# Optimization experiments

Hardware: AMD Instinct MI355X
Metric: run time of the kernel (lower is better)

## Reference

```python
import jax, jax.numpy as jnp
import numpy as np

EMBED_DIM = 128
NUM_SYMBOLS = 100000
PAD_IDX = NUM_SYMBOLS
B = 8192
K = 50


def setup_inputs() -> dict:
    key = jax.random.key(0)
    ks = jax.random.split(key, 10)
    emb = jax.random.normal(ks[0], (NUM_SYMBOLS + 1, EMBED_DIM), jnp.float32) * 0.02
    emb = emb.at[PAD_IDX].set(0.0)  # padding_idx row is zero
    xav2 = 1.0 / np.sqrt(0.5 * (2 * EMBED_DIM + EMBED_DIM))
    xavg1 = 1.0 / np.sqrt(0.5 * (EMBED_DIM + EMBED_DIM // 2))
    xavg2 = 1.0 / np.sqrt(0.5 * (EMBED_DIM // 2 + 1))
    return {
        "entity": jax.random.randint(ks[1], (B,), 0, NUM_SYMBOLS),
        "connections": jax.random.randint(ks[2], (B, K, 2), 0, NUM_SYMBOLS),
        "symbol_emb": emb,
        "gcn_w_W": jax.random.normal(ks[3], (EMBED_DIM, 2 * EMBED_DIM), jnp.float32) * xav2,
        "gcn_w_b": jnp.zeros((EMBED_DIM,), jnp.float32),
        "gcn_b": jnp.zeros((EMBED_DIM,), jnp.float32),
        "gate_w1": jax.random.normal(ks[4], (EMBED_DIM // 2, EMBED_DIM), jnp.float32) * xavg1,
        "gate_b1": jnp.zeros((EMBED_DIM // 2,), jnp.float32),
        "gate_w2": jax.random.normal(ks[5], (1, EMBED_DIM // 2), jnp.float32) * xavg2,
        "gate_b2": jnp.zeros((1,), jnp.float32),
        "gate_temp": jnp.float32(1.0),
    }


def reference(entity, connections, symbol_emb, gcn_w_W, gcn_w_b, gcn_b,
              gate_w1, gate_b1, gate_w2, gate_b2, gate_temp):
    # Gather: center + (relation, entity) neighbor embeddings
    self_emb = symbol_emb[entity]                      # [B, D]
    rel = symbol_emb[connections[..., 0]]              # [B, K, D]
    ent = symbol_emb[connections[..., 1]]              # [B, K, D]
    # Linear transform of concatenated (rel, ent): gcn_w
    nbr = jnp.einsum('bkf,df->bkd', jnp.concatenate([rel, ent], axis=-1), gcn_w_W) + gcn_w_b  # [B, K, D]
    # Similarity attention (scaled dot product with center embedding)
    scores = jnp.einsum('bd,bkd->bk', self_emb, nbr) / jnp.sqrt(jnp.float32(EMBED_DIM))
    attn = jax.nn.softmax(scores, axis=-1)             # [B, K]
    # Content-based gating MLP (D -> D/2 -> 1), temperature-scaled sigmoid
    h = jax.nn.relu(jnp.einsum('bkd,hd->bkh', nbr, gate_w1) + gate_b1)
    gate = jax.nn.sigmoid((jnp.einsum('bkh,oh->bko', h, gate_w2) + gate_b2) / gate_temp)  # [B, K, 1]
    # Weight neighbors, aggregate='max' over k_neighbors, bias + tanh
    weighted = attn[..., None] * gate * nbr            # [B, K, D]
    out = jnp.max(weighted, axis=1)                    # [B, D]
    return jnp.tanh(out + gcn_b)
```

## Files before the change

### kernel.cpp

```cpp
#include <hip/hip_runtime.h>

#define EMBED_D 128
#define KNBR 50
#define STR 136
#define NROWS 102
#define ZK 50
#define NTF 52
#define XSTR 264
#define NSTR 136
#define MROWS 64

typedef __attribute__((ext_vector_type(8))) short short8;
typedef __attribute__((ext_vector_type(4))) float floatx4;

__device__ __forceinline__ float b2f(unsigned short u) {
    union { unsigned int i; float f; } v;
    v.i = ((unsigned int)u) << 16;
    return v.f;
}
__device__ __forceinline__ unsigned short f2b(float f) {
    union { float f; unsigned int i; } v;
    v.f = f;
    return (unsigned short)((v.i + 0x7fffu + ((v.i >> 16) & 1u)) >> 16);
}

__device__ __forceinline__ float dpp_row_sum16(float v) {
    int y;
    y = __builtin_amdgcn_update_dpp(0, __builtin_bit_cast(int, v), 0xB1, 0xF, 0xF, true);
    v += __builtin_bit_cast(float, y);
    y = __builtin_amdgcn_update_dpp(0, __builtin_bit_cast(int, v), 0x4E, 0xF, 0xF, true);
    v += __builtin_bit_cast(float, y);
    y = __builtin_amdgcn_update_dpp(0, __builtin_bit_cast(int, v), 0x124, 0xF, 0xF, true);
    v += __builtin_bit_cast(float, y);
    y = __builtin_amdgcn_update_dpp(0, __builtin_bit_cast(int, v), 0x128, 0xF, 0xF, true);
    v += __builtin_bit_cast(float, y);
    return v;
}

__device__ __forceinline__ bool detect_bf16(const unsigned short* p) {
    float mx = 0.f;
#pragma unroll
    for (int i = 0; i < 64; ++i) {
        const float a = fabsf(b2f(p[i]));
        if (a < 3.0e38f && a > mx) mx = a;
    }
    return mx < 1.0f;
}


struct TinyTensors {
    const void* src[6];
    unsigned short* dst[6];
    int n[6];
};

__device__ __forceinline__ void conv_chunk(const void* src, unsigned short* dst,
                                           long i, bool isbf) {
    if (isbf) {
        *(short8*)(dst + i * 8) = *(const short8*)((const unsigned short*)src + i * 8);
    } else {
        const float* p = (const float*)src + i * 8;
        const floatx4 a = *(const floatx4*)p;
        const floatx4 c = *(const floatx4*)(p + 4);
        short8 r;
        r[0] = (short)f2b(a[0]); r[1] = (short)f2b(a[1]);
        r[2] = (short)f2b(a[2]); r[3] = (short)f2b(a[3]);
        r[4] = (short)f2b(c[0]); r[5] = (short)f2b(c[1]);
        r[6] = (short)f2b(c[2]); r[7] = (short)f2b(c[3]);
        *(short8*)(dst + i * 8) = r;
    }
}

__global__ void convert_all_kernel(const void* __restrict__ emb_src, unsigned short* __restrict__ emb_dst,
                                   long n8, int nEmb,
                                   const void* __restrict__ gw_src, unsigned short* __restrict__ gw_dst,
                                   long gw8,
                                   const void* __restrict__ w1_src, unsigned short* __restrict__ w1_dst,
                                   long w18,
                                   const void* __restrict__ gwb_src, const void* __restrict__ b1_src,
                                   unsigned short* __restrict__ wg_dst,
                                   float* __restrict__ bg_dst,
                                   int* __restrict__ flag_dst,
                                   TinyTensors tt) {
    __shared__ int isbfS;
    if (threadIdx.x == 0) isbfS = detect_bf16((const unsigned short*)emb_src) ? 1 : 0;
    __syncthreads();
    const bool isbf = (isbfS != 0);
    const int bid = blockIdx.x;

    if (bid < 64) {
        const int j = bid;
        const int f = threadIdx.x;
        float a = 0.f;
        if (isbf) {
            const unsigned short* w1u = (const unsigned short*)w1_src;
            const unsigned short* gwu = (const unsigned short*)gw_src;
            for (int d = 0; d < EMBED_D; ++d)
                a += b2f(w1u[j * EMBED_D + d]) * b2f(gwu[(long)d * 256 + f]);
        } else {
            const float* w1f = (const float*)w1_src;
            const float* gwf = (const float*)gw_src;
            for (int d = 0; d < EMBED_D; ++d)
                a += w1f[j * EMBED_D + d] * gwf[(long)d * 256 + f];
        }
        wg_dst[j * 256 + f] = f2b(a);
        if (f == 0) {
            float s = 0.f;
            if (isbf) {
                const unsigned short* w1u = (const unsigned short*)w1_src;
                const unsigned short* gu = (const unsigned short*)gwb_src;
                for (int d = 0; d < EMBED_D; ++d) s += b2f(w1u[j * EMBED_D + d]) * b2f(gu[d]);
                bg_dst[j] = s + b2f(((const unsigned short*)b1_src)[j]);
            } else {
                const float* w1f = (const float*)w1_src;
                const float* gf = (const float*)gwb_src;
                for (int d = 0; d < EMBED_D; ++d) s += w1f[j * EMBED_D + d] * gf[d];
                bg_dst[j] = s + ((const float*)b1_src)[j];
            }
        }
    } else if (bid == 64) {
        if (threadIdx.x == 0) *flag_dst = isbf ? 1 : 0;
#pragma unroll
        for (int ti = 0; ti < 6; ++ti) {
            const int n = tt.n[ti];
            for (int i = threadIdx.x; i < n; i += 256) {
                const float v = isbf ? b2f(((const unsigned short*)tt.src[ti])[i])
                                     : ((const float*)tt.src[ti])[i];
                tt.dst[ti][i] = f2b(v);
            }
        }
    } else if (bid < 85) {
        const long q = (long)(bid - 65) * 256 + threadIdx.x;
        if (q < gw8) conv_chunk(gw_src, gw_dst, q, isbf);
        else if (q < gw8 + w18) conv_chunk(w1_src, w1_dst, q - gw8, isbf);
    } else {
        const long i0 = (long)(bid - 85) * 512 + threadIdx.x;
        if (i0 < n8) conv_chunk(emb_src, emb_dst, i0, isbf);
        const long i1 = i0 + 256;
        if (i1 < n8) conv_chunk(emb_src, emb_dst, i1, isbf);
    }
}


__global__ __launch_bounds__(256, 5)
void embed_matcher_fast(const int* __restrict__ entity, const int* __restrict__ conn,
                        const unsigned short* __restrict__ emb,
                        const unsigned short* __restrict__ gw,
                        const unsigned short* __restrict__ wg,
                        const float* __restrict__ bgp,
                        const unsigned short* __restrict__ gwb,
                        const unsigned short* __restrict__ gcnb,
                        const unsigned short* __restrict__ w2,
                        const unsigned short* __restrict__ b2v,
                        const unsigned short* __restrict__ temp,
                        const int* __restrict__ flagp,
                        void* __restrict__ out)
{
    __shared__ __align__(16) unsigned short Xs[NROWS * STR];
    __shared__ __align__(16) float selfE[EMBED_D];
    __shared__ float scoresP[4 * MROWS];
    __shared__ float glP[4 * MROWS];
    __shared__ __align__(16) float attnS[MROWS];
    __shared__ int flagS;

    float* NsF = (float*)Xs;

    const int t = threadIdx.x;
    const int b = blockIdx.x;
    const int lane = t & 63;
    const int wave = t >> 6;
    const int l15 = lane & 15;
    const int quad = lane >> 4;
    const int cbase = b * (KNBR * 2);

    const int k3 = 48 + l15;
    const int rowk3 = (k3 < KNBR) ? k3 : ZK;

    floatx4 acc[4][3];
    const floatx4 fzero = {0.f, 0.f, 0.f, 0.f};
#pragma unroll
    for (int m = 0; m < 4; ++m)
#pragma unroll
        for (int T = 0; T < 3; ++T) acc[m][T] = fzero;

    {
        int syms[7];
#pragma unroll
        for (int i = 0; i < 7; ++i) {
            const int c = t + 256 * i;
            syms[i] = (c < KNBR * 2 * 16) ? conn[cbase + (c >> 4)] : 0;
        }
#pragma unroll
        for (int i = 0; i < 7; ++i) {
            const int c = t + 256 * i;
            if (c < KNBR * 2 * 16) {
                const short8 v = *(const short8*)(emb + (long)syms[i] * EMBED_D + (c & 15) * 8);
                *(short8*)(Xs + (c >> 4) * STR + (c & 15) * 8) = v;
            }
        }
        const short8 z8 = {0, 0, 0, 0, 0, 0, 0, 0};
        if (t < 34)
            *(short8*)(Xs + ZK * 2 * STR + t * 8) = z8;
        if (t < EMBED_D) selfE[t] = b2f(emb[(long)entity[b] * EMBED_D + t]);
        if (t == 0) flagS = *flagp;
    }
    __syncthreads();

    const unsigned short* gB0 = gw + (wave * 32 + l15) * 256;
    const unsigned short* gB1 = gB0 + 16 * 256;
    const unsigned short* gWg = wg + (wave * 16 + l15) * 256;

    short8 B0c = *(const short8*)(gB0 + quad * 8);
    short8 B1c = *(const short8*)(gB1 + quad * 8);
#pragma unroll
    for (int ft = 0; ft < 8; ++ft) {
        const short8 Bgc = *(const short8*)(gWg + ft * 32 + quad * 8);
        short8 B0n, B1n;
        if (ft < 7) {
            const int kn = (ft + 1) * 32 + quad * 8;
            B0n = *(const short8*)(gB0 + kn);
            B1n = *(const short8*)(gB1 + kn);
        }
        const int half = ft >> 2;
        const int cofs = (ft & 3) * 32 + quad * 8;
        short8 A[4];
#pragma unroll
        for (int m = 0; m < 3; ++m)
            A[m] = *(const short8*)(Xs + ((m * 16 + l15) * 2 + half) * STR + cofs);
        A[3] = *(const short8*)(Xs + (rowk3 * 2 + half) * STR + cofs);
#pragma unroll
        for (int m = 0; m < 4; ++m) {
            acc[m][0] = __builtin_amdgcn_mfma_f32_16x16x32_bf16(A[m], B0c, acc[m][0], 0, 0, 0);
            acc[m][1] = __builtin_amdgcn_mfma_f32_16x16x32_bf16(A[m], B1c, acc[m][1], 0, 0, 0);
            acc[m][2] = __builtin_amdgcn_mfma_f32_16x16x32_bf16(A[m], Bgc, acc[m][2], 0, 0, 0);
        }
        if (ft < 7) { B0c = B0n; B1c = B1n; }
    }
    __syncthreads();

    {
        const int dcol0 = wave * 32 + l15;
        const int dcol1 = dcol0 + 16;
        const float bias0 = b2f(gwb[dcol0]);
        const float bias1 = b2f(gwb[dcol1]);
        const float se0 = selfE[dcol0];
        const float se1 = selfE[dcol1];
        const float bgj = bgp[wave * 16 + l15];
        const float w2j = b2f(w2[wave * 16 + l15]);
#pragma unroll
        for (int m = 0; m < 4; ++m) {
            const int rbase = m * 16 + quad * 4;
            floatx4 v0, v1;
            float sc[4], gl[4];
#pragma unroll
            for (int r = 0; r < 4; ++r) {
                v0[r] = acc[m][0][r] + bias0;
                v1[r] = acc[m][1][r] + bias1;
                sc[r] = se0 * v0[r] + se1 * v1[r];
                gl[r] = fmaxf(acc[m][2][r] + bgj, 0.f) * w2j;
            }
            if (m < 3 || quad == 0) {
                *(floatx4*)(NsF + dcol0 * NTF + rbase) = v0;
                *(floatx4*)(NsF + dcol1 * NTF + rbase) = v1;
            }
#pragma unroll
            for (int r = 0; r < 4; ++r) {
                sc[r] = dpp_row_sum16(sc[r]);
                gl[r] = dpp_row_sum16(gl[r]);
            }
            const float sv = (l15 == 0) ? sc[0] : ((l15 == 1) ? sc[1] : ((l15 == 2) ? sc[2] : sc[3]));
            const float gv = (l15 == 0) ? gl[0] : ((l15 == 1) ? gl[1] : ((l15 == 2) ? gl[2] : gl[3]));
            if (l15 < 4) {
                scoresP[wave * MROWS + rbase + l15] = sv;
                glP[wave * MROWS + rbase + l15] = gv;
            }
        }
    }
    __syncthreads();

    if (t < 64) {
        const float ssum = scoresP[t] + scoresP[64 + t] + scoresP[128 + t] + scoresP[192 + t];
        const float s = (t < KNBR) ? ssum * 0.088388347648318447f : -INFINITY;
        float mx = s;
#pragma unroll
        for (int o = 32; o > 0; o >>= 1) mx = fmaxf(mx, __shfl_xor(mx, o));
        const float e = (t < KNBR) ? expf(s - mx) : 0.f;
        float sum = e;
#pragma unroll
        for (int o = 32; o > 0; o >>= 1) sum += __shfl_xor(sum, o);
        float a = e / sum;
        if (t < KNBR) {
            const float invT = 1.0f / b2f(temp[0]);
            const float logit = glP[t] + glP[64 + t] + glP[128 + t] + glP[192 + t] + b2f(b2v[0]);
            a *= 1.0f / (1.0f + expf(-logit * invT));
        }
        attnS[t] = a;
    }
    __syncthreads();

    if (t < EMBED_D) {
        const float* nr = NsF + t * NTF;
        float mx = -INFINITY;
#pragma unroll
        for (int c = 0; c < 12; ++c) {
            const floatx4 nv = *(const floatx4*)(nr + c * 4);
            const floatx4 av = *(const floatx4*)(attnS + c * 4);
#pragma unroll
            for (int j = 0; j < 4; ++j)
                mx = fmaxf(mx, av[j] * nv[j]);
        }
        mx = fmaxf(mx, attnS[48] * nr[48]);
        mx = fmaxf(mx, attnS[49] * nr[49]);
        const float o = tanhf(mx + b2f(gcnb[t]));
        if (flagS)
            ((unsigned short*)out)[(long)b * EMBED_D + t] = f2b(o);
        else
            ((float*)out)[(long)b * EMBED_D + t] = o;
    }
}


template <bool BF16IN>
__device__ __forceinline__ short8 load8g(const void* base, long off) {
    if constexpr (BF16IN) {
        return *(const short8*)((const unsigned short*)base + off);
    } else {
        const float* p = (const float*)base + off;
        const floatx4 a = *(const floatx4*)p;
        const floatx4 c = *(const floatx4*)(p + 4);
        short8 r;
        r[0] = (short)f2b(a[0]); r[1] = (short)f2b(a[1]);
        r[2] = (short)f2b(a[2]); r[3] = (short)f2b(a[3]);
        r[4] = (short)f2b(c[0]); r[5] = (short)f2b(c[1]);
        r[6] = (short)f2b(c[2]); r[7] = (short)f2b(c[3]);
        return r;
    }
}
template <bool BF16IN>
__device__ __forceinline__ float loadSg(const void* base, long off) {
    if constexpr (BF16IN) return b2f(((const unsigned short*)base)[off]);
    else return ((const float*)base)[off];
}

template <bool BF16IN>
__device__ __forceinline__ void body_fb(
    const int* entity, const int* conn, const void* emb, const void* gw,
    const void* gwb, const void* gcnb, const void* w1, const void* b1,
    const void* w2, const void* b2, const void* temp, void* out,
    unsigned short* Xs, unsigned short* Ns,
    float* selfE, float* scoresS, float* attnS, float* gsumS)
{
    const int t = threadIdx.x, b = blockIdx.x;
    const int lane = t & 63, wave = t >> 6, l15 = lane & 15, quad = lane >> 4;
    short8 Bfrag[8][2];
#pragma unroll
    for (int ft = 0; ft < 8; ++ft)
#pragma unroll
        for (int nn = 0; nn < 2; ++nn)
            Bfrag[ft][nn] = load8g<BF16IN>(gw, (wave * 32 + nn * 16 + l15) * 256 + ft * 32 + quad * 8);
    short8 W1frag[4];
#pragma unroll
    for (int ft = 0; ft < 4; ++ft)
        W1frag[ft] = load8g<BF16IN>(w1, (wave * 16 + l15) * 128 + ft * 32 + quad * 8);
    const float b1j = loadSg<BF16IN>(b1, wave * 16 + l15);
    const float w2j = loadSg<BF16IN>(w2, wave * 16 + l15);
    {
        const int cbase = b * (KNBR * 2);
        for (int c = t; c < KNBR * 2 * 16; c += 256) {
            const int r = c >> 4, j = c & 15;
            const int sym = conn[cbase + r];
            *(short8*)(Xs + (r >> 1) * XSTR + (r & 1) * 128 + j * 8) =
                load8g<BF16IN>(emb, (long)sym * EMBED_D + j * 8);
        }
        for (int i = t; i < (MROWS - KNBR) * 256; i += 256)
            Xs[(KNBR + (i >> 8)) * XSTR + (i & 255)] = 0;
        if (t < EMBED_D) selfE[t] = loadSg<BF16IN>(emb, (long)entity[b] * EMBED_D + t);
        if (t < MROWS) gsumS[t] = loadSg<BF16IN>(b2, 0);
    }
    __syncthreads();
    floatx4 acc[4][2];
    const floatx4 fzero = {0.f, 0.f, 0.f, 0.f};
#pragma unroll
    for (int m = 0; m < 4; ++m)
#pragma unroll
        for (int nn = 0; nn < 2; ++nn) acc[m][nn] = fzero;
#pragma unroll
    for (int ft = 0; ft < 8; ++ft) {
        short8 A[4];
#pragma unroll
        for (int m = 0; m < 4; ++m)
            A[m] = *(const short8*)(Xs + (m * 16 + l15) * XSTR + ft * 32 + quad * 8);
#pragma unroll
        for (int m = 0; m < 4; ++m)
#pragma unroll
            for (int nn = 0; nn < 2; ++nn)
                acc[m][nn] = __builtin_amdgcn_mfma_f32_16x16x32_bf16(A[m], Bfrag[ft][nn], acc[m][nn], 0, 0, 0);
    }
#pragma unroll
    for (int nn = 0; nn < 2; ++nn) {
        const int dcol = wave * 32 + nn * 16 + l15;
        const float bias = loadSg<BF16IN>(gwb, dcol);
#pragma unroll
        for (int m = 0; m < 4; ++m)
#pragma unroll
            for (int r = 0; r < 4; ++r)
                Ns[(m * 16 + quad * 4 + r) * NSTR + dcol] = f2b(acc[m][nn][r] + bias);
    }
    __syncthreads();
    {
        const int k = t >> 2, q = t & 3;
        float p = 0.f;
        if (k < KNBR) {
            const unsigned short* nr = Ns + k * NSTR + q * 32;
            const float* se = selfE + q * 32;
#pragma unroll
            for (int i = 0; i < 32; ++i) p += se[i] * b2f(nr[i]);
        }
        p += __shfl_xor(p, 1);
        p += __shfl_xor(p, 2);
        if (k < KNBR && q == 0) scoresS[k] = p * 0.088388347648318447f;
    }
    __syncthreads();
    if (t < 64) {
        const float s = (t < KNBR) ? scoresS[t] : -INFINITY;
        float mx = s;
#pragma unroll
        for (int o = 32; o > 0; o >>= 1) mx = fmaxf(mx, __shfl_xor(mx, o));
        const float e = (t < KNBR) ? expf(s - mx) : 0.f;
        float sum = e;
#pragma unroll
        for (int o = 32; o > 0; o >>= 1) sum += __shfl_xor(sum, o);
        attnS[t] = e / sum;
    }
    floatx4 acc2[4];
#pragma unroll
    for (int m = 0; m < 4; ++m) acc2[m] = fzero;
#pragma unroll
    for (int ft = 0; ft < 4; ++ft) {
        short8 A2[4];
#pragma unroll
        for (int m = 0; m < 4; ++m)
            A2[m] = *(const short8*)(Ns + (m * 16 + l15) * NSTR + ft * 32 + quad * 8);
#pragma unroll
        for (int m = 0; m < 4; ++m)
            acc2[m] = __builtin_amdgcn_mfma_f32_16x16x32_bf16(A2[m], W1frag[ft], acc2[m], 0, 0, 0);
    }
#pragma unroll
    for (int m = 0; m < 4; ++m)
#pragma unroll
        for (int r = 0; r < 4; ++r) {
            float c = fmaxf(acc2[m][r] + b1j, 0.f) * w2j;
            c += __shfl_xor(c, 1); c += __shfl_xor(c, 2);
            c += __shfl_xor(c, 4); c += __shfl_xor(c, 8);
            if (l15 == 0) atomicAdd(&gsumS[m * 16 + quad * 4 + r], c);
        }
    __syncthreads();
    if (t < KNBR) {
        const float invT = 1.0f / loadSg<BF16IN>(temp, 0);
        attnS[t] *= 1.0f / (1.0f + expf(-gsumS[t] * invT));
    }
    __syncthreads();
    if (t < EMBED_D) {
        float mx = -INFINITY;
        for (int k = 0; k < KNBR; ++k)
            mx = fmaxf(mx, attnS[k] * b2f(Ns[k * NSTR + t]));
        const float o = tanhf(mx + loadSg<BF16IN>(gcnb, t));
        if constexpr (BF16IN)
            ((unsigned short*)out)[(long)b * EMBED_D + t] = f2b(o);
        else
            ((float*)out)[(long)b * EMBED_D + t] = o;
    }
}

__global__ __launch_bounds__(256, 2)
void embed_matcher_fallback(const int* entity, const int* conn, const void* emb,
                            const void* gw, const void* gwb, const void* gcnb,
                            const void* w1, const void* b1, const void* w2,
                            const void* b2, const void* temp, void* out)
{
    __shared__ __align__(16) unsigned short Xs[MROWS * XSTR];
    __shared__ __align__(16) unsigned short Ns[MROWS * NSTR];
    __shared__ float selfE[EMBED_D];
    __shared__ float scoresS[MROWS];
    __shared__ float attnS[MROWS];
    __shared__ float gsumS[MROWS];
    if (detect_bf16((const unsigned short*)emb))
        body_fb<true>(entity, conn, emb, gw, gwb, gcnb, w1, b1, w2, b2, temp, out,
                      Xs, Ns, selfE, scoresS, attnS, gsumS);
    else
        body_fb<false>(entity, conn, emb, gw, gwb, gcnb, w1, b1, w2, b2, temp, out,
                       Xs, Ns, selfE, scoresS, attnS, gsumS);
}


static inline size_t align256(size_t x) { return (x + 255) & ~(size_t)255; }

extern "C" void kernel_launch(void* const* d_in, const int* in_sizes, int n_in,
                              void* d_out, int out_size, void* d_ws, size_t ws_size,
                              hipStream_t stream) {
    (void)n_in; (void)out_size;
    const int B = in_sizes[0];

    const long n_emb = in_sizes[2];
    size_t off[9], cur = 0;
    const int ns[8] = {in_sizes[3], in_sizes[4], in_sizes[5], in_sizes[6],
                       in_sizes[7], in_sizes[8], in_sizes[9], in_sizes[10]};
    off[0] = 0; cur = align256((size_t)n_emb * 2);
    for (int i = 0; i < 8; ++i) { off[i + 1] = cur; cur = align256(cur + (size_t)ns[i] * 2); }
    const size_t off_wg = cur; cur = align256(cur + 64 * 256 * 2);
    const size_t off_bg = cur; cur = align256(cur + 64 * 4);
    const size_t off_fl = cur; cur = align256(cur + 4);

    if (ws_size < cur) {
        embed_matcher_fallback<<<B, 256, 0, stream>>>(
            (const int*)d_in[0], (const int*)d_in[1],
            d_in[2], d_in[3], d_in[4], d_in[5],
            d_in[6], d_in[7], d_in[8], d_in[9], d_in[10], d_out);
        return;
    }

    char* ws = (char*)d_ws;
    unsigned short* emb_b = (unsigned short*)(ws + off[0]);

    TinyTensors tt;
    const int tin[6] = {4, 5, 7, 8, 9, 10};
    for (int i = 0; i < 6; ++i) {
        tt.src[i] = d_in[tin[i]];
        tt.dst[i] = (unsigned short*)(ws + off[tin[i] - 2]);
        tt.n[i] = in_sizes[tin[i]];
    }

    const long n8 = n_emb / 8;
    const int nEmb = (int)((n8 + 511) / 512);
    const long gw8 = in_sizes[3] / 8;
    const long w18 = in_sizes[6] / 8;
    convert_all_kernel<<<85 + nEmb, 256, 0, stream>>>(
        d_in[2], emb_b, n8, nEmb,
        d_in[3], (unsigned short*)(ws + off[1]), gw8,
        d_in[6], (unsigned short*)(ws + off[4]), w18,
        d_in[4], d_in[7],
        (unsigned short*)(ws + off_wg),
        (float*)(ws + off_bg),
        (int*)(ws + off_fl),
        tt);

    embed_matcher_fast<<<B, 256, 0, stream>>>(
        (const int*)d_in[0], (const int*)d_in[1],
        emb_b,
        (const unsigned short*)(ws + off[1]),
        (const unsigned short*)(ws + off_wg),
        (const float*)(ws + off_bg),
        (const unsigned short*)(ws + off[2]),
        (const unsigned short*)(ws + off[3]),
        (const unsigned short*)(ws + off[6]),
        (const unsigned short*)(ws + off[7]),
        (const unsigned short*)(ws + off[8]),
        (const int*)(ws + off_fl),
        d_out);
}
```

Measured before the change: 233.0 us.

## Gather embeddings directly into LDS with XOR-swizzled layout

Replaces register-staged global-to-LDS copies of the gathered embedding rows with direct global_load_lds transfers. The padded row stride is replaced by a 128-element row with an XOR swizzle on the 16-byte chunk index to avoid bank conflicts when reading MFMA operands. The first weight loads move ahead of the barrier, and s_setprio wraps the MFMA block. The aim is to cut VGPR pressure and the latency of the gather, at the cost of depending on the lane-to-LDS address pattern of the direct-load builtin being correct.

```diff
diff --git a/kernel.cpp b/kernel.cpp
--- a/kernel.cpp
+++ b/kernel.cpp
@@ -2,7 +2,6 @@
 
 #define EMBED_D 128
 #define KNBR 50
-#define STR 136
 #define NROWS 102
 #define ZK 50
 #define NTF 52
@@ -156,14 +155,14 @@
                         const int* __restrict__ flagp,
                         void* __restrict__ out)
 {
-    __shared__ __align__(16) unsigned short Xs[NROWS * STR];
+    __shared__ __align__(16) float NsF[128 * NTF];
     __shared__ __align__(16) float selfE[EMBED_D];
     __shared__ float scoresP[4 * MROWS];
     __shared__ float glP[4 * MROWS];
     __shared__ __align__(16) float attnS[MROWS];
     __shared__ int flagS;
 
-    float* NsF = (float*)Xs;
+    unsigned short* Xs = (unsigned short*)NsF;
 
     const int t = threadIdx.x;
     const int b = blockIdx.x;
@@ -187,24 +186,29 @@
         int syms[7];
 #pragma unroll
         for (int i = 0; i < 7; ++i) {
-            const int c = t + 256 * i;
-            syms[i] = (c < KNBR * 2 * 16) ? conn[cbase + (c >> 4)] : 0;
+            const int g = 4 * i + wave;
+            const int r = g * 4 + (lane >> 4);
+            syms[i] = (g < 25) ? conn[cbase + r] : 0;
         }
 #pragma unroll
         for (int i = 0; i < 7; ++i) {
-            const int c = t + 256 * i;
-            if (c < KNBR * 2 * 16) {
-                const short8 v = *(const short8*)(emb + (long)syms[i] * EMBED_D + (c & 15) * 8);
-                *(short8*)(Xs + (c >> 4) * STR + (c & 15) * 8) = v;
+            const int g = 4 * i + wave;
+            if (g < 25) {
+                const int r = g * 4 + (lane >> 4);
+                const int j = l15 ^ (r & 15);
+                const unsigned short* gp = emb + (long)syms[i] * EMBED_D + j * 8;
+                __builtin_amdgcn_global_load_lds(
+                    (const __attribute__((address_space(1))) void*)gp,
+                    (__attribute__((address_space(3))) void*)(Xs + g * 4 * 128),
+                    16, 0, 0);
             }
         }
         const short8 z8 = {0, 0, 0, 0, 0, 0, 0, 0};
-        if (t < 34)
-            *(short8*)(Xs + ZK * 2 * STR + t * 8) = z8;
+        if (t < 32)
+            *(short8*)(Xs + 100 * 128 + t * 8) = z8;
         if (t < EMBED_D) selfE[t] = b2f(emb[(long)entity[b] * EMBED_D + t]);
         if (t == 0) flagS = *flagp;
     }
-    __syncthreads();
 
     const unsigned short* gB0 = gw + (wave * 32 + l15) * 256;
     const unsigned short* gB1 = gB0 + 16 * 256;
@@ -212,6 +216,9 @@
 
     short8 B0c = *(const short8*)(gB0 + quad * 8);
     short8 B1c = *(const short8*)(gB1 + quad * 8);
+
+    __syncthreads();
+
 #pragma unroll
     for (int ft = 0; ft < 8; ++ft) {
         const short8 Bgc = *(const short8*)(gWg + ft * 32 + quad * 8);
@@ -222,18 +229,25 @@
             B1n = *(const short8*)(gB1 + kn);
         }
         const int half = ft >> 2;
-        const int cofs = (ft & 3) * 32 + quad * 8;
+        const int jc = (ft & 3) * 4 + quad;
         short8 A[4];
 #pragma unroll
-        for (int m = 0; m < 3; ++m)
-            A[m] = *(const short8*)(Xs + ((m * 16 + l15) * 2 + half) * STR + cofs);
-        A[3] = *(const short8*)(Xs + (rowk3 * 2 + half) * STR + cofs);
+        for (int m = 0; m < 3; ++m) {
+            const int r = (m * 16 + l15) * 2 + half;
+            A[m] = *(const short8*)(Xs + r * 128 + ((jc ^ (r & 15)) << 3));
+        }
+        {
+            const int r = rowk3 * 2 + half;
+            A[3] = *(const short8*)(Xs + r * 128 + ((jc ^ (r & 15)) << 3));
+        }
+        __builtin_amdgcn_s_setprio(1);
 #pragma unroll
         for (int m = 0; m < 4; ++m) {
             acc[m][0] = __builtin_amdgcn_mfma_f32_16x16x32_bf16(A[m], B0c, acc[m][0], 0, 0, 0);
             acc[m][1] = __builtin_amdgcn_mfma_f32_16x16x32_bf16(A[m], B1c, acc[m][1], 0, 0, 0);
             acc[m][2] = __builtin_amdgcn_mfma_f32_16x16x32_bf16(A[m], Bgc, acc[m][2], 0, 0, 0);
         }
+        __builtin_amdgcn_s_setprio(0);
         if (ft < 7) { B0c = B0n; B1c = B1n; }
     }
     __syncthreads();
```

New measurement: 266.5 us. +14.4%, slower.

## Make matcher kernel persistent with double-buffered gather prefetch and register-resident weights

Applied to the files above, without the earlier changes.

Replaces the one-block-per-item launch with 512 persistent blocks that each loop over 16 items. While the MFMA stage runs on the current item, the next item's embedding rows are gathered into registers and then written into a second LDS buffer. Connection indices are fetched two items ahead. The GCN and gate weight fragments are loaded once into registers and reused across items. The aim is to hide gather latency and cut repeated weight loads, at the cost of higher register and LDS use, which lowers occupancy (launch bounds drop from 5 to 2).

```diff
diff --git a/kernel.cpp b/kernel.cpp
--- a/kernel.cpp
+++ b/kernel.cpp
@@ -142,8 +142,8 @@
 }
 
 
-__global__ __launch_bounds__(256, 5)
-void embed_matcher_fast(const int* __restrict__ entity, const int* __restrict__ conn,
+__global__ __launch_bounds__(256, 2)
+void embed_matcher_pipe(const int* __restrict__ entity, const int* __restrict__ conn,
                         const unsigned short* __restrict__ emb,
                         const unsigned short* __restrict__ gw,
                         const unsigned short* __restrict__ wg,
@@ -154,168 +154,227 @@
                         const unsigned short* __restrict__ b2v,
                         const unsigned short* __restrict__ temp,
                         const int* __restrict__ flagp,
-                        void* __restrict__ out)
+                        void* __restrict__ out,
+                        int nItems)
 {
-    __shared__ __align__(16) unsigned short Xs[NROWS * STR];
-    __shared__ __align__(16) float selfE[EMBED_D];
+    __shared__ __align__(16) unsigned short buf[2][NROWS * STR];
+    __shared__ int connS[2][2 * KNBR];
+    __shared__ int eS[2];
+    __shared__ __align__(16) float selfE[2][EMBED_D];
     __shared__ float scoresP[4 * MROWS];
     __shared__ float glP[4 * MROWS];
     __shared__ __align__(16) float attnS[MROWS];
-    __shared__ int flagS;
-
-    float* NsF = (float*)Xs;
 
     const int t = threadIdx.x;
-    const int b = blockIdx.x;
     const int lane = t & 63;
     const int wave = t >> 6;
     const int l15 = lane & 15;
     const int quad = lane >> 4;
-    const int cbase = b * (KNBR * 2);
+    const int i0 = blockIdx.x * nItems;
 
     const int k3 = 48 + l15;
     const int rowk3 = (k3 < KNBR) ? k3 : ZK;
 
-    floatx4 acc[4][3];
-    const floatx4 fzero = {0.f, 0.f, 0.f, 0.f};
-#pragma unroll
-    for (int m = 0; m < 4; ++m)
-#pragma unroll
-        for (int T = 0; T < 3; ++T) acc[m][T] = fzero;
-
+    const int dcol0 = wave * 32 + l15;
+    const int dcol1 = dcol0 + 16;
+    const float bias0 = b2f(gwb[dcol0]);
+    const float bias1 = b2f(gwb[dcol1]);
+    const float bgj = bgp[wave * 16 + l15];
+    const float w2j = b2f(w2[wave * 16 + l15]);
+    const float invT = 1.0f / b2f(temp[0]);
+    const float b2b = b2f(b2v[0]);
+    const float gcb = (t < EMBED_D) ? b2f(gcnb[t]) : 0.f;
+    const int flag = *flagp;
+
+    short8 Bf0[8], Bf1[8], Bfg[8];
     {
-        int syms[7];
-#pragma unroll
-        for (int i = 0; i < 7; ++i) {
-            const int c = t + 256 * i;
-            syms[i] = (c < KNBR * 2 * 16) ? conn[cbase + (c >> 4)] : 0;
-        }
+        const unsigned short* gB0 = gw + (wave * 32 + l15) * 256;
+        const unsigned short* gB1 = gB0 + 16 * 256;
+        const unsigned short* gWg = wg + (wave * 16 + l15) * 256;
+#pragma unroll
+        for (int ft = 0; ft < 8; ++ft) {
+            Bf0[ft] = *(const short8*)(gB0 + ft * 32 + quad * 8);
+            Bf1[ft] = *(const short8*)(gB1 + ft * 32 + quad * 8);
+            Bfg[ft] = *(const short8*)(gWg + ft * 32 + quad * 8);
+        }
+    }
+
+    {
+        int c0 = 0, c1 = 0;
+        if (t < 2 * KNBR) {
+            c0 = conn[(long)i0 * (2 * KNBR) + t];
+            if (nItems > 1) c1 = conn[(long)(i0 + 1) * (2 * KNBR) + t];
+        }
+        int e0 = 0, e1 = 0;
+        if (t == 0) {
+            e0 = entity[i0];
+            if (nItems > 1) e1 = entity[i0 + 1];
+        }
+        const short8 z8 = {0, 0, 0, 0, 0, 0, 0, 0};
+        if (t < 34) {
+            *(short8*)(buf[0] + ZK * 2 * STR + t * 8) = z8;
+            *(short8*)(buf[1] + ZK * 2 * STR + t * 8) = z8;
+        }
+        if (t < 2 * KNBR) { connS[0][t] = c0; connS[1][t] = c1; }
+        if (t == 0) { eS[0] = e0; eS[1] = e1; }
+    }
+    __syncthreads();
+
+    short8 g[7];
+    unsigned short sEv = 0;
+    {
 #pragma unroll
         for (int i = 0; i < 7; ++i) {
             const int c = t + 256 * i;
             if (c < KNBR * 2 * 16) {
-                const short8 v = *(const short8*)(emb + (long)syms[i] * EMBED_D + (c & 15) * 8);
-                *(short8*)(Xs + (c >> 4) * STR + (c & 15) * 8) = v;
-            }
-        }
-        const short8 z8 = {0, 0, 0, 0, 0, 0, 0, 0};
-        if (t < 34)
-            *(short8*)(Xs + ZK * 2 * STR + t * 8) = z8;
-        if (t < EMBED_D) selfE[t] = b2f(emb[(long)entity[b] * EMBED_D + t]);
-        if (t == 0) flagS = *flagp;
-    }
-    __syncthreads();
-
-    const unsigned short* gB0 = gw + (wave * 32 + l15) * 256;
-    const unsigned short* gB1 = gB0 + 16 * 256;
-    const unsigned short* gWg = wg + (wave * 16 + l15) * 256;
-
-    short8 B0c = *(const short8*)(gB0 + quad * 8);
-    short8 B1c = *(const short8*)(gB1 + quad * 8);
-#pragma unroll
-    for (int ft = 0; ft < 8; ++ft) {
-        const short8 Bgc = *(const short8*)(gWg + ft * 32 + quad * 8);
-        short8 B0n, B1n;
-        if (ft < 7) {
-            const int kn = (ft + 1) * 32 + quad * 8;
-            B0n = *(const short8*)(gB0 + kn);
-            B1n = *(const short8*)(gB1 + kn);
-        }
-        const int half = ft >> 2;
-        const int cofs = (ft & 3) * 32 + quad * 8;
-        short8 A[4];
-#pragma unroll
-        for (int m = 0; m < 3; ++m)
-            A[m] = *(const short8*)(Xs + ((m * 16 + l15) * 2 + half) * STR + cofs);
-        A[3] = *(const short8*)(Xs + (rowk3 * 2 + half) * STR + cofs);
-#pragma unroll
-        for (int m = 0; m < 4; ++m) {
-            acc[m][0] = __builtin_amdgcn_mfma_f32_16x16x32_bf16(A[m], B0c, acc[m][0], 0, 0, 0);
-            acc[m][1] = __builtin_amdgcn_mfma_f32_16x16x32_bf16(A[m], B1c, acc[m][1], 0, 0, 0);
-            acc[m][2] = __builtin_amdgcn_mfma_f32_16x16x32_bf16(A[m], Bgc, acc[m][2], 0, 0, 0);
-        }
-        if (ft < 7) { B0c = B0n; B1c = B1n; }
-    }
-    __syncthreads();
-
+                const int sym = connS[0][c >> 4];
+                g[i] = *(const short8*)(emb + (long)sym * EMBED_D + (c & 15) * 8);
+            }
+        }
+        if (t < EMBED_D) sEv = emb[(long)eS[0] * EMBED_D + t];
+    }
+    __syncthreads();
     {
-        const int dcol0 = wave * 32 + l15;
-        const int dcol1 = dcol0 + 16;
-        const float bias0 = b2f(gwb[dcol0]);
-        const float bias1 = b2f(gwb[dcol1]);
-        const float se0 = selfE[dcol0];
-        const float se1 = selfE[dcol1];
-        const float bgj = bgp[wave * 16 + l15];
-        const float w2j = b2f(w2[wave * 16 + l15]);
-#pragma unroll
-        for (int m = 0; m < 4; ++m) {
-            const int rbase = m * 16 + quad * 4;
-            floatx4 v0, v1;
-            float sc[4], gl[4];
-#pragma unroll
-            for (int r = 0; r < 4; ++r) {
-                v0[r] = acc[m][0][r] + bias0;
-                v1[r] = acc[m][1][r] + bias1;
-                sc[r] = se0 * v0[r] + se1 * v1[r];
-                gl[r] = fmaxf(acc[m][2][r] + bgj, 0.f) * w2j;
-            }
-            if (m < 3 || quad == 0) {
-                *(floatx4*)(NsF + dcol0 * NTF + rbase) = v0;
-                *(floatx4*)(NsF + dcol1 * NTF + rbase) = v1;
-            }
-#pragma unroll
-            for (int r = 0; r < 4; ++r) {
-                sc[r] = dpp_row_sum16(sc[r]);
-                gl[r] = dpp_row_sum16(gl[r]);
-            }
-            const float sv = (l15 == 0) ? sc[0] : ((l15 == 1) ? sc[1] : ((l15 == 2) ? sc[2] : sc[3]));
-            const float gv = (l15 == 0) ? gl[0] : ((l15 == 1) ? gl[1] : ((l15 == 2) ? gl[2] : gl[3]));
-            if (l15 < 4) {
-                scoresP[wave * MROWS + rbase + l15] = sv;
-                glP[wave * MROWS + rbase + l15] = gv;
-            }
-        }
-    }
-    __syncthreads();
-
-    if (t < 64) {
-        const float ssum = scoresP[t] + scoresP[64 + t] + scoresP[128 + t] + scoresP[192 + t];
-        const float s = (t < KNBR) ? ssum * 0.088388347648318447f : -INFINITY;
-        float mx = s;
-#pragma unroll
-        for (int o = 32; o > 0; o >>= 1) mx = fmaxf(mx, __shfl_xor(mx, o));
-        const float e = (t < KNBR) ? expf(s - mx) : 0.f;
-        float sum = e;
-#pragma unroll
-        for (int o = 32; o > 0; o >>= 1) sum += __shfl_xor(sum, o);
-        float a = e / sum;
-        if (t < KNBR) {
-            const float invT = 1.0f / b2f(temp[0]);
-            const float logit = glP[t] + glP[64 + t] + glP[128 + t] + glP[192 + t] + b2f(b2v[0]);
-            a *= 1.0f / (1.0f + expf(-logit * invT));
-        }
-        attnS[t] = a;
-    }
-    __syncthreads();
-
-    if (t < EMBED_D) {
-        const float* nr = NsF + t * NTF;
-        float mx = -INFINITY;
-#pragma unroll
-        for (int c = 0; c < 12; ++c) {
-            const floatx4 nv = *(const floatx4*)(nr + c * 4);
-            const floatx4 av = *(const floatx4*)(attnS + c * 4);
-#pragma unroll
-            for (int j = 0; j < 4; ++j)
-                mx = fmaxf(mx, av[j] * nv[j]);
-        }
-        mx = fmaxf(mx, attnS[48] * nr[48]);
-        mx = fmaxf(mx, attnS[49] * nr[49]);
-        const float o = tanhf(mx + b2f(gcnb[t]));
-        if (flagS)
-            ((unsigned short*)out)[(long)b * EMBED_D + t] = f2b(o);
-        else
-            ((float*)out)[(long)b * EMBED_D + t] = o;
+#pragma unroll
+        for (int i = 0; i < 7; ++i) {
+            const int c = t + 256 * i;
+            if (c < KNBR * 2 * 16)
+                *(short8*)(buf[0] + (c >> 4) * STR + (c & 15) * 8) = g[i];
+        }
+        if (t < EMBED_D) selfE[0][t] = b2f(sEv);
+    }
+
+    const floatx4 fzero = {0.f, 0.f, 0.f, 0.f};
+
+    for (int it = 0; it < nItems; ++it) {
+        const int cur = it & 1, nxt = cur ^ 1;
+        __syncthreads();
+
+        int cReg = 0, eReg = 0;
+        if (it + 2 < nItems) {
+            if (t < 2 * KNBR) cReg = conn[(long)(i0 + it + 2) * (2 * KNBR) + t];
+            if (t == 0) eReg = entity[i0 + it + 2];
+        }
+        if (it + 1 < nItems) {
+#pragma unroll
+            for (int i = 0; i < 7; ++i) {
+                const int c = t + 256 * i;
+                if (c < KNBR * 2 * 16) {
+                    const int sym = connS[nxt][c >> 4];
+                    g[i] = *(const short8*)(emb + (long)sym * EMBED_D + (c & 15) * 8);
+                }
+            }
+            if (t < EMBED_D) sEv = emb[(long)eS[nxt] * EMBED_D + t];
+        }
+
+        const unsigned short* Xs = buf[cur];
+        floatx4 acc[4][3];
+#pragma unroll
+        for (int m = 0; m < 4; ++m)
+#pragma unroll
+            for (int T = 0; T < 3; ++T) acc[m][T] = fzero;
+#pragma unroll
+        for (int ft = 0; ft < 8; ++ft) {
+            const int half = ft >> 2;
+            const int cofs = (ft & 3) * 32 + quad * 8;
+#pragma unroll
+            for (int m = 0; m < 4; ++m) {
+                const int rr = (m < 3) ? (m * 16 + l15) : rowk3;
+                const short8 Am = *(const short8*)(Xs + (rr * 2 + half) * STR + cofs);
+                acc[m][0] = __builtin_amdgcn_mfma_f32_16x16x32_bf16(Am, Bf0[ft], acc[m][0], 0, 0, 0);
+                acc[m][1] = __builtin_amdgcn_mfma_f32_16x16x32_bf16(Am, Bf1[ft], acc[m][1], 0, 0, 0);
+                acc[m][2] = __builtin_amdgcn_mfma_f32_16x16x32_bf16(Am, Bfg[ft], acc[m][2], 0, 0, 0);
+            }
+        }
+        __syncthreads();
+
+        if (it + 1 < nItems) {
+#pragma unroll
+            for (int i = 0; i < 7; ++i) {
+                const int c = t + 256 * i;
+                if (c < KNBR * 2 * 16)
+                    *(short8*)(buf[nxt] + (c >> 4) * STR + (c & 15) * 8) = g[i];
+            }
+            if (t < EMBED_D) selfE[nxt][t] = b2f(sEv);
+        }
+        if (it + 2 < nItems) {
+            if (t < 2 * KNBR) connS[cur][t] = cReg;
+            if (t == 0) eS[cur] = eReg;
+        }
+
+        float* NsF = (float*)buf[cur];
+        {
+            const float se0 = selfE[cur][dcol0];
+            const float se1 = selfE[cur][dcol1];
+#pragma unroll
+            for (int m = 0; m < 4; ++m) {
+                const int rbase = m * 16 + quad * 4;
+                floatx4 v0, v1;
+                float sc[4], gl[4];
+#pragma unroll
+                for (int r = 0; r < 4; ++r) {
+                    v0[r] = acc[m][0][r] + bias0;
+                    v1[r] = acc[m][1][r] + bias1;
+                    sc[r] = se0 * v0[r] + se1 * v1[r];
+                    gl[r] = fmaxf(acc[m][2][r] + bgj, 0.f) * w2j;
+                }
+                if (m < 3 || quad == 0) {
+                    *(floatx4*)(NsF + dcol0 * NTF + rbase) = v0;
+                    *(floatx4*)(NsF + dcol1 * NTF + rbase) = v1;
+                }
+#pragma unroll
+                for (int r = 0; r < 4; ++r) {
+                    sc[r] = dpp_row_sum16(sc[r]);
+                    gl[r] = dpp_row_sum16(gl[r]);
+                }
+                const float sv = (l15 == 0) ? sc[0] : ((l15 == 1) ? sc[1] : ((l15 == 2) ? sc[2] : sc[3]));
+                const float gv = (l15 == 0) ? gl[0] : ((l15 == 1) ? gl[1] : ((l15 == 2) ? gl[2] : gl[3]));
+                if (l15 < 4) {
+                    scoresP[wave * MROWS + rbase + l15] = sv;
+                    glP[wave * MROWS + rbase + l15] = gv;
+                }
+            }
+        }
+        __syncthreads();
+
+        if (t < 64) {
+            const float ssum = scoresP[t] + scoresP[64 + t] + scoresP[128 + t] + scoresP[192 + t];
+            const float s = (t < KNBR) ? ssum * 0.088388347648318447f : -INFINITY;
+            float mx = s;
+#pragma unroll
+            for (int o = 32; o > 0; o >>= 1) mx = fmaxf(mx, __shfl_xor(mx, o));
+            const float e = (t < KNBR) ? expf(s - mx) : 0.f;
+            float sum = e;
+#pragma unroll
+            for (int o = 32; o > 0; o >>= 1) sum += __shfl_xor(sum, o);
+            float a = e / sum;
+            if (t < KNBR) {
+                const float logit = glP[t] + glP[64 + t] + glP[128 + t] + glP[192 + t] + b2b;
+                a *= 1.0f / (1.0f + expf(-logit * invT));
+            }
+            attnS[t] = a;
+        }
+        __syncthreads();
+
+        if (t < EMBED_D) {
+            const float* nr = NsF + t * NTF;
+            float mx = -INFINITY;
+#pragma unroll
+            for (int c = 0; c < 12; ++c) {
+                const floatx4 nv = *(const floatx4*)(nr + c * 4);
+                const floatx4 av = *(const floatx4*)(attnS + c * 4);
+#pragma unroll
+                for (int j = 0; j < 4; ++j)
+                    mx = fmaxf(mx, av[j] * nv[j]);
+            }
+            mx = fmaxf(mx, attnS[48] * nr[48]);
+            mx = fmaxf(mx, attnS[49] * nr[49]);
+            const float o = tanhf(mx + gcb);
+            if (flag)
+                ((unsigned short*)out)[(long)(i0 + it) * EMBED_D + t] = f2b(o);
+            else
+                ((float*)out)[(long)(i0 + it) * EMBED_D + t] = o;
+        }
     }
 }
 
@@ -544,7 +603,11 @@
         (int*)(ws + off_fl),
         tt);
 
-    embed_matcher_fast<<<B, 256, 0, stream>>>(
+    int nblk, nit;
+    if (B % 512 == 0 && B >= 1024) { nblk = 512; nit = B / 512; }
+    else { nblk = B; nit = 1; }
+
+    embed_matcher_pipe<<<nblk, 256, 0, stream>>>(
         (const int*)d_in[0], (const int*)d_in[1],
         emb_b,
         (const unsigned short*)(ws + off[1]),
@@ -556,5 +619,6 @@
         (const unsigned short*)(ws + off[7]),
         (const unsigned short*)(ws + off[8]),
         (const int*)(ws + off_fl),
-        d_out);
-}
+        d_out,
+        nit);
+}
```

Result: slower. 238.1 us (+2.2%).
